# Optimization experiments

Hardware: AMD Instinct MI355X
Metric: run time of the kernel (lower is better)

The kernel has to match this reference:

```python
import jax, jax.numpy as jnp
import numpy as np

B, S = 32, 48
H, W_IMG, DEPTH = 48, 72, 1
UNITS, MOTOR, SENSORY = 48, 4, 1283
ODE_UNFOLDS = 6
N_ACTIONS = 2
EPS = 1e-8


def setup_inputs() -> dict:
    key = jax.random.key(0)
    ks = jax.random.split(key, 32)
    inp = {}
    inp["image"] = jax.random.uniform(ks[0], (B, S, DEPTH, H, W_IMG), jnp.float32)
    inp["rel_pos"] = jax.random.normal(ks[1], (B, S, 3), jnp.float32)
    # CNN params: channels [1->32->64->32], k=3, stride=2, VALID
    dims = [DEPTH, 32, 64, 32]
    for i in range(3):
        fan_in = dims[i] * 9
        inp[f"w{i}"] = jax.random.normal(ks[2 + i], (dims[i + 1], dims[i], 3, 3), jnp.float32) / np.sqrt(fan_in)
        inp[f"b{i}"] = jnp.zeros((dims[i + 1],), jnp.float32)
    # LTC input affine mapping
    inp["input_w"] = jnp.ones((SENSORY,), jnp.float32)
    inp["input_b"] = jnp.zeros((SENSORY,), jnp.float32)
    # LTC neuron params (ncps default init ranges)
    u = lambda k, shp, lo, hi: jax.random.uniform(k, shp, jnp.float32, lo, hi)
    inp["gleak"] = u(ks[6], (UNITS,), 0.001, 1.0)
    inp["vleak"] = u(ks[7], (UNITS,), -0.2, 0.2)
    inp["cm"] = u(ks[8], (UNITS,), 0.4, 0.6)
    # recurrent synapse params [pre=UNITS, post=UNITS]
    inp["sigma"] = u(ks[9], (UNITS, UNITS), 3.0, 8.0)
    inp["mu"] = u(ks[10], (UNITS, UNITS), 0.3, 0.8)
    inp["w_syn"] = u(ks[11], (UNITS, UNITS), 0.001, 1.0)
    inp["erev"] = (2.0 * jax.random.randint(ks[12], (UNITS, UNITS), 0, 2).astype(jnp.float32) - 1.0)
    # sensory synapse params [pre=SENSORY, post=UNITS]
    inp["s_sigma"] = u(ks[13], (SENSORY, UNITS), 3.0, 8.0)
    inp["s_mu"] = u(ks[14], (SENSORY, UNITS), 0.3, 0.8)
    inp["s_w"] = u(ks[15], (SENSORY, UNITS), 0.001, 1.0)
    inp["s_erev"] = (2.0 * jax.random.randint(ks[16], (SENSORY, UNITS), 0, 2).astype(jnp.float32) - 1.0)
    # output affine mapping over the 4 motor neurons
    inp["w_out"] = jnp.ones((MOTOR,), jnp.float32)
    inp["b_out"] = jnp.zeros((MOTOR,), jnp.float32)
    # actor head: Linear(4 -> n_actions) + tanh
    inp["w_head"] = jax.random.normal(ks[17], (MOTOR, N_ACTIONS), jnp.float32) / np.sqrt(MOTOR)
    inp["b_head"] = jnp.zeros((N_ACTIONS,), jnp.float32)
    # sparsity masks (buffers, non-trainable): AutoNCP-like sparse wiring
    inp["syn_mask"] = jax.random.randint(ks[18], (UNITS, UNITS), 0, 2, jnp.int32)
    inp["sens_mask"] = (jax.random.uniform(ks[19], (SENSORY, UNITS)) < 0.4).astype(jnp.int32)
    return inp


def _cnn(x, w0, b0, w1, b1, w2, b2):
    # x: [N, C, H, W], VALID padding, stride 2, ReLU
    for w, b in ((w0, b0), (w1, b1), (w2, b2)):
        x = jax.lax.conv_general_dilated(x, w, (2, 2), "VALID",
                                         dimension_numbers=("NCHW", "OIHW", "NCHW"))
        x = jax.nn.relu(x + b[None, :, None, None])
    return x


def _ltc(xs, input_w, input_b, gleak, vleak, cm, sigma, mu, w_syn, erev,
         s_sigma, s_mu, s_w, s_erev, w_out, b_out, syn_mask_f, sens_mask_f):
    # xs: [B, S, SENSORY] -> outputs [B, S, MOTOR]
    xs = xs * input_w + input_b  # input affine mapping
    cm_t = cm * ODE_UNFOLDS      # cm / (elapsed_time / ode_unfolds), elapsed=1

    def cell(v, x_t):
        # sensory synapse activation, computed once per step: [B, SENSORY, UNITS]
        sa = s_w * jax.nn.sigmoid((x_t[:, :, None] - s_mu) * s_sigma) * sens_mask_f
        w_num_s = jnp.sum(sa * s_erev, axis=1)  # [B, UNITS]
        w_den_s = jnp.sum(sa, axis=1)
        for _ in range(ODE_UNFOLDS):
            # recurrent synapse activation: [B, UNITS(pre), UNITS(post)]
            wa = w_syn * jax.nn.sigmoid((v[:, :, None] - mu) * sigma) * syn_mask_f
            num = cm_t * v + gleak * vleak + jnp.sum(wa * erev, axis=1) + w_num_s
            den = cm_t + gleak + jnp.sum(wa, axis=1) + w_den_s + EPS
            v = num / den
        out = v[:, :MOTOR] * w_out + b_out  # motor neurons + output affine
        return v, out

    v0 = jnp.zeros((xs.shape[0], UNITS), xs.dtype)
    _, outs = jax.lax.scan(cell, v0, jnp.swapaxes(xs, 0, 1))  # scan over time
    return jnp.swapaxes(outs, 0, 1)  # [B, S, MOTOR]


def reference(image, rel_pos, w0, b0, w1, b1, w2, b2, input_w, input_b,
              gleak, vleak, cm, sigma, mu, w_syn, erev,
              s_sigma, s_mu, s_w, s_erev, w_out, b_out, w_head, b_head,
              syn_mask, sens_mask):
    b, s = image.shape[0], image.shape[1]
    img = image.reshape(b * s, *image.shape[2:])
    feat = _cnn(img, w0, b0, w1, b1, w2, b2).reshape(b, s, -1)  # [B,S,1280]
    x = jnp.concatenate([feat, rel_pos.reshape(b, s, -1)], axis=2)  # [B,S,1283]
    outs = _ltc(x, input_w, input_b, gleak, vleak, cm, sigma, mu, w_syn, erev,
                s_sigma, s_mu, s_w, s_erev, w_out, b_out,
                syn_mask.astype(x.dtype), sens_mask.astype(x.dtype))
    pooled = outs.mean(axis=1)  # [B, MOTOR]
    return jnp.tanh(pooled @ w_head + b_head)  # [B, N_ACTIONS]
```

## Files before the change

kernel.cpp:

```cpp
#include <hip/hip_runtime.h>
#include <math.h>

#define DINL __device__ __forceinline__

typedef __attribute__((ext_vector_type(8))) short short8;
typedef __attribute__((ext_vector_type(4))) float f32x4;
typedef unsigned short ushortx;
typedef unsigned int uintx;


static constexpr int O_OUT2 = 0;
static constexpr int O_X    = O_OUT2 + 1536 * 187 * 64;
static constexpr int O_WNUM = O_X + 1536 * 1283;
static constexpr int O_WDEN = O_WNUM + 1536 * 48;
static constexpr int O_SP4  = O_WDEN + 1536 * 48;
static constexpr int O_WM   = O_SP4 + 4 * 48 * 1283;
static constexpr int O_WME  = O_WM + 48 * 48;
static constexpr int O_W2T  = O_WME + 48 * 48;
static constexpr int O_W1H  = O_W2T + 32 * 9 * 64;
static constexpr int O_W1L  = O_W1H + 9216;
static constexpr int O_R4   = O_W1L + 9216;

DINL float sigmoid_f(float z) {
  return __builtin_amdgcn_rcpf(1.f + __expf(-z));
}

DINL ushortx bf16_rne(float x) {
  uintx u = __float_as_uint(x);
  return (ushortx)((u + 0x7FFFu + ((u >> 16) & 1u)) >> 16);
}

__global__ __launch_bounds__(256) void k_pre(
    const float* __restrict__ ssig, const float* __restrict__ smu,
    const float* __restrict__ sw, const float* __restrict__ serev,
    const int* __restrict__ smask,
    const float* __restrict__ w_syn, const float* __restrict__ erev,
    const int* __restrict__ syn_mask,
    const float* __restrict__ gmu, const float* __restrict__ gsig,
    const float* __restrict__ w1, const float* __restrict__ w2,
    float4* __restrict__ o_p4, float4* __restrict__ o_r4,
    float* __restrict__ w2t, ushortx* __restrict__ w1h, ushortx* __restrict__ w1l) {
  const int bid = blockIdx.x, t = threadIdx.x;
  if (bid < 241) {
    int idx = bid * 256 + t;
    if (idx < 61584) {
      int i = idx / 48, j = idx - i * 48;
      float m = (float)smask[idx];
      float w = sw[idx] * m;
      o_p4[j * 1283 + i] = make_float4(ssig[idx], smu[idx], w, w * serev[idx]);
    }
  } else if (bid < 250) {
    int idx = (bid - 241) * 256 + t;
    if (idx < 2304) {
      float wm = w_syn[idx] * (float)syn_mask[idx];
      o_r4[idx] = make_float4(gmu[idx], gsig[idx], wm, wm * erev[idx]);
    }
  } else {
    int idx = (bid - 250) * 256 + t;
    if (idx < 18432) {
      int oc = idx / 288;
      int rem = idx - oc * 288;
      int c = rem / 9, k = rem - c * 9;
      float v = w1[idx];
      ushortx h = bf16_rne(v);
      float hv = __uint_as_float(((uintx)h) << 16);
      ushortx l = bf16_rne(v - hv);
      int dst = (k * 64 + oc) * 32 + c;
      w1h[dst] = h;
      w1l[dst] = l;
    } else if (idx < 36864) {
      int i2 = idx - 18432;
      int oc = i2 / 576;
      int rem = i2 - oc * 576;
      int c = rem / 9, k = rem - c * 9;
      w2t[(((oc & 15) * 9 + k) * 64 + c) * 2 + (oc >> 4)] = w2[i2];
    }
  }
}

__global__ __launch_bounds__(512) void k_conv12(const float* __restrict__ gimg,
        const float* __restrict__ w0, const float* __restrict__ b0,
        const ushortx* __restrict__ w1h, const ushortx* __restrict__ w1l,
        const float* __restrict__ b1, float* __restrict__ gout2) {
  extern __shared__ __align__(16) char dyn[];
  ushortx* c1h = (ushortx*)dyn;
  ushortx* c1l = c1h + 26496;
  float* smem_a = (float*)(c1l + 26496);
  float* sw0 = smem_a + 3456;
  float* sb0 = sw0 + 288;
  ushortx* swh = (ushortx*)smem_a;
  ushortx* swl = swh + 2048;

  const int n = blockIdx.x, t = threadIdx.x;

  const float* gi = gimg + n * 3456;
  for (int k = t; k < 3456; k += 512) smem_a[k] = gi[k];
  if (t < 288) sw0[t] = w0[t];
  if (t >= 480) sb0[t - 480] = b0[t - 480];

  const int lane = t & 63, wid = t >> 6;
  const int r15 = lane & 15, kg = lane >> 4;
  const int mt0 = (wid & 1) * 2;
  const int nt0 = (wid >> 1) * 3;
  int bbase[3], spv[3];
#pragma unroll
  for (int ni = 0; ni < 3; ++ni) {
    int sp = (nt0 + ni) * 16 + r15;
    spv[ni] = sp;
    int spc = sp > 186 ? 186 : sp;
    int oh = spc / 17, ow = spc - oh * 17;
    bbase[ni] = ((2 * oh) * 36 + 2 * ow) * 32 + kg * 8;
  }
  int aoff0 = (mt0 * 16 + r15) * 32 + kg * 8;
  float4 bb[2];
  bb[0] = *(const float4*)(b1 + mt0 * 16 + kg * 4);
  bb[1] = *(const float4*)(b1 + (mt0 + 1) * 16 + kg * 4);
  f32x4 acc[2][3];
#pragma unroll
  for (int mi = 0; mi < 2; ++mi)
#pragma unroll
    for (int ni = 0; ni < 3; ++ni) acc[mi][ni] = (f32x4)(0.f);

  __syncthreads();

  for (int idx = t; idx < 25760; idx += 512) {
    int c = idx & 31, sp = idx >> 5;
    int oh = sp / 35, ow = sp - oh * 35;
    const float* ip = smem_a + (2 * oh) * 72 + 2 * ow;
    const float* wp = sw0 + c * 9;
    float a = sb0[c];
#pragma unroll
    for (int kh = 0; kh < 3; ++kh)
      a += ip[kh * 72 + 0] * wp[kh * 3 + 0] + ip[kh * 72 + 1] * wp[kh * 3 + 1]
         + ip[kh * 72 + 2] * wp[kh * 3 + 2];
    a = fmaxf(a, 0.f);
    ushortx h = bf16_rne(a);
    float hv = __uint_as_float(((uintx)h) << 16);
    ushortx l = bf16_rne(a - hv);
    int pos = (oh * 36 + ow) * 32 + c;
    c1h[pos] = h;
    c1l[pos] = l;
  }

  const uintx* gwh = (const uintx*)w1h;
  const uintx* gwl = (const uintx*)w1l;
  for (int tap = 0; tap < 9; ++tap) {
    __syncthreads();
    for (int k = t; k < 1024; k += 512) {
      ((uintx*)swh)[k] = gwh[tap * 1024 + k];
      ((uintx*)swl)[k] = gwl[tap * 1024 + k];
    }
    __syncthreads();
    const int kh = tap / 3, kw = tap - kh * 3;
    const int toff = (kh * 36 + kw) * 32;
    short8 ah[2], al[2];
    ah[0] = *(const short8*)(swh + aoff0);
    al[0] = *(const short8*)(swl + aoff0);
    ah[1] = *(const short8*)(swh + aoff0 + 512);
    al[1] = *(const short8*)(swl + aoff0 + 512);
#pragma unroll
    for (int ni = 0; ni < 3; ++ni) {
      short8 bh = *(const short8*)(c1h + bbase[ni] + toff);
      short8 bl = *(const short8*)(c1l + bbase[ni] + toff);
#pragma unroll
      for (int mi = 0; mi < 2; ++mi) {
        acc[mi][ni] = __builtin_amdgcn_mfma_f32_16x16x32_bf16(ah[mi], bh, acc[mi][ni], 0, 0, 0);
        acc[mi][ni] = __builtin_amdgcn_mfma_f32_16x16x32_bf16(al[mi], bh, acc[mi][ni], 0, 0, 0);
        acc[mi][ni] = __builtin_amdgcn_mfma_f32_16x16x32_bf16(ah[mi], bl, acc[mi][ni], 0, 0, 0);
      }
    }
  }

  float* go = gout2 + n * 11968;
#pragma unroll
  for (int mi = 0; mi < 2; ++mi)
#pragma unroll
    for (int ni = 0; ni < 3; ++ni) {
      if (spv[ni] < 187) {
        float4 v;
        v.x = fmaxf(acc[mi][ni][0] + bb[mi].x, 0.f);
        v.y = fmaxf(acc[mi][ni][1] + bb[mi].y, 0.f);
        v.z = fmaxf(acc[mi][ni][2] + bb[mi].z, 0.f);
        v.w = fmaxf(acc[mi][ni][3] + bb[mi].w, 0.f);
        *(float4*)(go + spv[ni] * 64 + (mt0 + mi) * 16 + kg * 4) = v;
      }
    }
}

__global__ __launch_bounds__(256, 4) void k_conv3(const float* __restrict__ gout2,
        const float* __restrict__ w2t, const float* __restrict__ b2,
        const float* __restrict__ grel, float* __restrict__ gx) {
  __shared__ __align__(16) float sin2g[16 * 198];
  __shared__ __align__(16) float sw2g[16 * 290];
  const int n = blockIdx.x, t = threadIdx.x;
  const float* gi = gout2 + n * 11968;

  const int oc = t & 15, g = t >> 4;
  float acc[3][2];
  int rowb[3];
#pragma unroll
  for (int q = 0; q < 3; ++q) {
    acc[q][0] = b2[oc]; acc[q][1] = b2[oc + 16];
    int sp = q * 16 + g; if (sp > 39) sp = 39;
    int oh = sp >> 3, ow = sp & 7;
    rowb[q] = (2 * oh) * 18 + 2 * ow;
  }

  for (int grp = 0; grp < 4; ++grp) {
    for (int idx = t; idx < 2992; idx += 256) {
      int sp = idx >> 4, c = idx & 15;
      int h = sp / 17, w = sp - h * 17;
      sin2g[c * 198 + h * 18 + w] = gi[sp * 64 + grp * 16 + c];
    }
    for (int idx = t; idx < 4608; idx += 256) {
      int ocq2 = idx / 288, r = idx - ocq2 * 288;
      int k = r >> 5;
      sw2g[ocq2 * 290 + r] = w2t[(ocq2 * 9 + k) * 128 + grp * 32 + (r & 31)];
    }
    __syncthreads();

    for (int c = 0; c < 16; ++c) {
      const float* cb = sin2g + c * 198;
      const float* wb = sw2g + oc * 290 + c * 2;
#pragma unroll
      for (int kh = 0; kh < 3; ++kh) {
        float2 wv0 = *(const float2*)(wb + (kh * 3 + 0) * 32);
        float2 wv1 = *(const float2*)(wb + (kh * 3 + 1) * 32);
        float2 wv2 = *(const float2*)(wb + (kh * 3 + 2) * 32);
#pragma unroll
        for (int q = 0; q < 3; ++q) {
          const float* p = cb + rowb[q] + kh * 18;
          float2 x01 = *(const float2*)p;
          float x2 = p[2];
          acc[q][0] += x01.x * wv0.x + x01.y * wv1.x + x2 * wv2.x;
          acc[q][1] += x01.x * wv0.y + x01.y * wv1.y + x2 * wv2.y;
        }
      }
    }
    __syncthreads();
  }

  float* xo = gx + n * 1283;
#pragma unroll
  for (int q = 0; q < 3; ++q) {
    int sp = q * 16 + g;
    if (sp < 40) {
      xo[oc * 40 + sp]        = fmaxf(acc[q][0], 0.f);
      xo[(oc + 16) * 40 + sp] = fmaxf(acc[q][1], 0.f);
    }
  }
  if (t < 3) xo[1280 + t] = grel[n * 3 + t];
}

__global__ __launch_bounds__(256) void k_sensory(const float* __restrict__ gx,
        const float* __restrict__ iw, const float* __restrict__ ib,
        const float4* __restrict__ p4,
        float* __restrict__ wnum, float* __restrict__ wden) {
  __shared__ float xs[4 * 1283];
  const int t = threadIdx.x, bid = blockIdx.x;
  const int bs0 = (bid >> 1) * 4;
  const int jbase = (bid & 1) * 24;
  for (int idx = t; idx < 4 * 1283; idx += 256) {
    int slot = idx / 1283, i = idx - slot * 1283;
    xs[idx] = gx[(bs0 + slot) * 1283 + i] * iw[i] + ib[i];
  }
  __syncthreads();
  const int w = t >> 6, l = t & 63;
  for (int jj = 0; jj < 6; ++jj) {
    int j = jbase + w * 6 + jj;
    const float4* pp = p4 + j * 1283;
    float an[4], ad[4];
#pragma unroll
    for (int s2 = 0; s2 < 4; ++s2) { an[s2] = 0.f; ad[s2] = 0.f; }
    for (int i = l; i < 1283; i += 64) {
      float4 P = pp[i];
#pragma unroll
      for (int s2 = 0; s2 < 4; ++s2) {
        float sg = sigmoid_f((xs[s2 * 1283 + i] - P.y) * P.x);
        an[s2] += P.w * sg;
        ad[s2] += P.z * sg;
      }
    }
#pragma unroll
    for (int off = 32; off; off >>= 1)
#pragma unroll
      for (int s2 = 0; s2 < 4; ++s2) {
        an[s2] += __shfl_xor(an[s2], off);
        ad[s2] += __shfl_xor(ad[s2], off);
      }
    if (l == 0) {
#pragma unroll
      for (int s2 = 0; s2 < 4; ++s2) {
        wnum[(bs0 + s2) * 48 + j] = an[s2];
        wden[(bs0 + s2) * 48 + j] = ad[s2];
      }
    }
  }
}

__global__ __launch_bounds__(192) void k_scan(const float4* __restrict__ r4,
        const float* __restrict__ wnum, const float* __restrict__ wden,
        const float* __restrict__ gleak, const float* __restrict__ vleak,
        const float* __restrict__ cm,
        const float* __restrict__ w_out, const float* __restrict__ b_out,
        const float* __restrict__ w_head, const float* __restrict__ b_head,
        float* __restrict__ out) {
  __shared__ float swn[48 * 48], swd[48 * 48];
  __shared__ __align__(16) float vbuf[2][48];
  __shared__ float m4[4];
  const int t = threadIdx.x, b = blockIdx.x;
  const int j = t >> 2, g = t & 3;

  const float* gn = wnum + b * 2304;
  const float* gd = wden + b * 2304;
  for (int k = t; k < 2304; k += 192) { swn[k] = gn[k]; swd[k] = gd[k]; }

  float4 P[12];
#pragma unroll
  for (int q = 0; q < 12; ++q) P[q] = r4[(g * 12 + q) * 48 + j];

  const float cmt = cm[j] * 6.f;
  const float gl = gleak[j];
  const float glv = gl * vleak[j];
  if (t < 48) { vbuf[0][t] = 0.f; vbuf[1][t] = 0.f; }
  float psum = 0.f;
  __syncthreads();

  int cur = 0;
  for (int s = 0; s < 48; ++s) {
    float wns = swn[s * 48 + j], wds = swd[s * 48 + j];
#pragma unroll 1
    for (int u = 0; u < 6; ++u) {
      const float4* vb4 = (const float4*)&vbuf[cur][g * 12];
      float4 va = vb4[0], vb = vb4[1], vc = vb4[2];
      float vv[12] = {va.x, va.y, va.z, va.w, vb.x, vb.y, vb.z, vb.w,
                      vc.x, vc.y, vc.z, vc.w};
      float an = 0.f, ad = 0.f;
#pragma unroll
      for (int q = 0; q < 12; ++q) {
        float sg = sigmoid_f((vv[q] - P[q].x) * P[q].y);
        an += P[q].w * sg;
        ad += P[q].z * sg;
      }
      an += __shfl_xor(an, 1); ad += __shfl_xor(ad, 1);
      an += __shfl_xor(an, 2); ad += __shfl_xor(ad, 2);
      if (g == 0) {
        float vj = vbuf[cur][j];
        float num = cmt * vj + glv + an + wns;
        float den = cmt + gl + ad + wds + 1e-8f;
        vbuf[cur ^ 1][j] = num / den;
      }
      __syncthreads();
      cur ^= 1;
    }
    if (g == 0 && j < 4) psum += vbuf[cur][j];
  }
  if (g == 0 && j < 4) m4[j] = psum * (1.f / 48.f) * w_out[j] + b_out[j];
  __syncthreads();
  if (t < 2) {
    float a = b_head[t];
#pragma unroll
    for (int jm = 0; jm < 4; ++jm) a += m4[jm] * w_head[jm * 2 + t];
    out[b * 2 + t] = tanhf(a);
  }
}

extern "C" void kernel_launch(void* const* d_in, const int* in_sizes, int n_in,
                              void* d_out, int out_size, void* d_ws, size_t ws_size,
                              hipStream_t stream) {
  const float* image   = (const float*)d_in[0];
  const float* rel     = (const float*)d_in[1];
  const float* w0      = (const float*)d_in[2];
  const float* b0      = (const float*)d_in[3];
  const float* w1      = (const float*)d_in[4];
  const float* b1      = (const float*)d_in[5];
  const float* w2      = (const float*)d_in[6];
  const float* b2      = (const float*)d_in[7];
  const float* iw      = (const float*)d_in[8];
  const float* ib      = (const float*)d_in[9];
  const float* gleak   = (const float*)d_in[10];
  const float* vleak   = (const float*)d_in[11];
  const float* cm      = (const float*)d_in[12];
  const float* sigma   = (const float*)d_in[13];
  const float* mu      = (const float*)d_in[14];
  const float* w_syn   = (const float*)d_in[15];
  const float* erev    = (const float*)d_in[16];
  const float* s_sigma = (const float*)d_in[17];
  const float* s_mu    = (const float*)d_in[18];
  const float* s_w     = (const float*)d_in[19];
  const float* s_erev  = (const float*)d_in[20];
  const float* w_out   = (const float*)d_in[21];
  const float* b_out   = (const float*)d_in[22];
  const float* w_head  = (const float*)d_in[23];
  const float* b_head  = (const float*)d_in[24];
  const int* syn_mask  = (const int*)d_in[25];
  const int* sens_mask = (const int*)d_in[26];
  float* ws  = (float*)d_ws;
  float* out = (float*)d_out;

  hipFuncSetAttribute((const void*)k_conv12,
                      hipFuncAttributeMaxDynamicSharedMemorySize, 131072);

  k_pre<<<394, 256, 0, stream>>>(s_sigma, s_mu, s_w, s_erev, sens_mask,
      w_syn, erev, syn_mask, mu, sigma, w1, w2,
      (float4*)(ws + O_SP4), (float4*)(ws + O_R4), ws + O_W2T,
      (ushortx*)(ws + O_W1H), (ushortx*)(ws + O_W1L));

  k_conv12<<<1536, 512, 121088, stream>>>(image, w0, b0,
      (const ushortx*)(ws + O_W1H), (const ushortx*)(ws + O_W1L), b1, ws + O_OUT2);
  k_conv3<<<1536, 256, 0, stream>>>(ws + O_OUT2, ws + O_W2T, b2, rel, ws + O_X);

  k_sensory<<<768, 256, 0, stream>>>(ws + O_X, iw, ib,
      (const float4*)(ws + O_SP4), ws + O_WNUM, ws + O_WDEN);

  k_scan<<<32, 192, 0, stream>>>((const float4*)(ws + O_R4),
      ws + O_WNUM, ws + O_WDEN, gleak, vleak, cm,
      w_out, b_out, w_head, b_head, out);
}
```

Baseline: 512.0 us.

## Fuse conv3 into CNN kernel with split-bf16 MFMA and single-wave scan

Conv3 is merged into the conv1/conv2 kernel. The conv2 output stays in LDS as hi/lo bf16 pairs and is consumed by a split-bf16 MFMA conv3, so the global round trip of the large intermediate is gone. LDS indexing is XOR-swizzled to reduce bank conflicts, and conv2 weights are now read straight from global memory instead of being staged per tap. The LTC scan is rewritten to use one wavefront per batch, passing state through shuffles instead of LDS and barriers, which trades per-step sync cost for more work per thread and a possible accuracy change from the 3-term bf16 split.

```diff
diff --git a/kernel.cpp b/kernel.cpp
--- a/kernel.cpp
+++ b/kernel.cpp
@@ -4,22 +4,21 @@
 #define DINL __device__ __forceinline__
 
 typedef __attribute__((ext_vector_type(8))) short short8;
+typedef __attribute__((ext_vector_type(4))) short short4x;
 typedef __attribute__((ext_vector_type(4))) float f32x4;
 typedef unsigned short ushortx;
 typedef unsigned int uintx;
 
 
-static constexpr int O_OUT2 = 0;
-static constexpr int O_X    = O_OUT2 + 1536 * 187 * 64;
+static constexpr int O_X    = 0;
 static constexpr int O_WNUM = O_X + 1536 * 1283;
 static constexpr int O_WDEN = O_WNUM + 1536 * 48;
 static constexpr int O_SP4  = O_WDEN + 1536 * 48;
-static constexpr int O_WM   = O_SP4 + 4 * 48 * 1283;
-static constexpr int O_WME  = O_WM + 48 * 48;
-static constexpr int O_W2T  = O_WME + 48 * 48;
-static constexpr int O_W1H  = O_W2T + 32 * 9 * 64;
+static constexpr int O_W1H  = O_SP4 + 4 * 48 * 1283;
 static constexpr int O_W1L  = O_W1H + 9216;
-static constexpr int O_R4   = O_W1L + 9216;
+static constexpr int O_W3H  = O_W1L + 9216;
+static constexpr int O_W3L  = O_W3H + 9216;
+static constexpr int O_R4   = O_W3L + 9216;
 
 DINL float sigmoid_f(float z) {
   return __builtin_amdgcn_rcpf(1.f + __expf(-z));
@@ -29,6 +28,8 @@
   uintx u = __float_as_uint(x);
   return (ushortx)((u + 0x7FFFu + ((u >> 16) & 1u)) >> 16);
 }
+
+DINL int swz(int sp, int idx) { return idx ^ (((sp >> 1) & 7) << 3); }
 
 __global__ __launch_bounds__(256) void k_pre(
     const float* __restrict__ ssig, const float* __restrict__ smu,
@@ -39,7 +40,8 @@
     const float* __restrict__ gmu, const float* __restrict__ gsig,
     const float* __restrict__ w1, const float* __restrict__ w2,
     float4* __restrict__ o_p4, float4* __restrict__ o_r4,
-    float* __restrict__ w2t, ushortx* __restrict__ w1h, ushortx* __restrict__ w1l) {
+    ushortx* __restrict__ w1h, ushortx* __restrict__ w1l,
+    ushortx* __restrict__ w3h, ushortx* __restrict__ w3l) {
   const int bid = blockIdx.x, t = threadIdx.x;
   if (bid < 241) {
     int idx = bid * 256 + t;
@@ -66,35 +68,42 @@
       float hv = __uint_as_float(((uintx)h) << 16);
       ushortx l = bf16_rne(v - hv);
       int dst = (k * 64 + oc) * 32 + c;
-      w1h[dst] = h;
-      w1l[dst] = l;
+      w1h[dst] = h; w1l[dst] = l;
     } else if (idx < 36864) {
       int i2 = idx - 18432;
       int oc = i2 / 576;
       int rem = i2 - oc * 576;
       int c = rem / 9, k = rem - c * 9;
-      w2t[(((oc & 15) * 9 + k) * 64 + c) * 2 + (oc >> 4)] = w2[i2];
-    }
-  }
-}
-
-__global__ __launch_bounds__(512) void k_conv12(const float* __restrict__ gimg,
+      float v = w2[i2];
+      ushortx h = bf16_rne(v);
+      float hv = __uint_as_float(((uintx)h) << 16);
+      ushortx l = bf16_rne(v - hv);
+      int dst = (k * 32 + oc) * 64 + c;
+      w3h[dst] = h; w3l[dst] = l;
+    }
+  }
+}
+
+__global__ __launch_bounds__(512) void k_cnn(const float* __restrict__ gimg,
         const float* __restrict__ w0, const float* __restrict__ b0,
         const ushortx* __restrict__ w1h, const ushortx* __restrict__ w1l,
-        const float* __restrict__ b1, float* __restrict__ gout2) {
+        const float* __restrict__ b1,
+        const ushortx* __restrict__ w3h, const ushortx* __restrict__ w3l,
+        const float* __restrict__ b2,
+        const float* __restrict__ grel, float* __restrict__ gx) {
   extern __shared__ __align__(16) char dyn[];
   ushortx* c1h = (ushortx*)dyn;
   ushortx* c1l = c1h + 26496;
-  float* smem_a = (float*)(c1l + 26496);
-  float* sw0 = smem_a + 3456;
+  float* simg = (float*)(c1l + 26496);
+  float* sw0 = simg + 3456;
   float* sb0 = sw0 + 288;
-  ushortx* swh = (ushortx*)smem_a;
-  ushortx* swl = swh + 2048;
+  ushortx* o2h = c1h;
+  ushortx* o2l = c1l;
 
   const int n = blockIdx.x, t = threadIdx.x;
 
   const float* gi = gimg + n * 3456;
-  for (int k = t; k < 3456; k += 512) smem_a[k] = gi[k];
+  for (int k = t; k < 3456; k += 512) simg[k] = gi[k];
   if (t < 288) sw0[t] = w0[t];
   if (t >= 480) sb0[t - 480] = b0[t - 480];
 
@@ -102,16 +111,15 @@
   const int r15 = lane & 15, kg = lane >> 4;
   const int mt0 = (wid & 1) * 2;
   const int nt0 = (wid >> 1) * 3;
-  int bbase[3], spv[3];
+  int b36[3], spv[3];
 #pragma unroll
   for (int ni = 0; ni < 3; ++ni) {
     int sp = (nt0 + ni) * 16 + r15;
     spv[ni] = sp;
     int spc = sp > 186 ? 186 : sp;
     int oh = spc / 17, ow = spc - oh * 17;
-    bbase[ni] = ((2 * oh) * 36 + 2 * ow) * 32 + kg * 8;
-  }
-  int aoff0 = (mt0 * 16 + r15) * 32 + kg * 8;
+    b36[ni] = (2 * oh) * 36 + 2 * ow;
+  }
   float4 bb[2];
   bb[0] = *(const float4*)(b1 + mt0 * 16 + kg * 4);
   bb[1] = *(const float4*)(b1 + (mt0 + 1) * 16 + kg * 4);
@@ -126,7 +134,7 @@
   for (int idx = t; idx < 25760; idx += 512) {
     int c = idx & 31, sp = idx >> 5;
     int oh = sp / 35, ow = sp - oh * 35;
-    const float* ip = smem_a + (2 * oh) * 72 + 2 * ow;
+    const float* ip = simg + (2 * oh) * 72 + 2 * ow;
     const float* wp = sw0 + c * 9;
     float a = sb0[c];
 #pragma unroll
@@ -137,31 +145,28 @@
     ushortx h = bf16_rne(a);
     float hv = __uint_as_float(((uintx)h) << 16);
     ushortx l = bf16_rne(a - hv);
-    int pos = (oh * 36 + ow) * 32 + c;
+    int sp36 = oh * 36 + ow;
+    int pos = swz(sp36, sp36 * 32 + c);
     c1h[pos] = h;
     c1l[pos] = l;
   }
-
-  const uintx* gwh = (const uintx*)w1h;
-  const uintx* gwl = (const uintx*)w1l;
+  __syncthreads();
+
   for (int tap = 0; tap < 9; ++tap) {
-    __syncthreads();
-    for (int k = t; k < 1024; k += 512) {
-      ((uintx*)swh)[k] = gwh[tap * 1024 + k];
-      ((uintx*)swl)[k] = gwl[tap * 1024 + k];
-    }
-    __syncthreads();
     const int kh = tap / 3, kw = tap - kh * 3;
-    const int toff = (kh * 36 + kw) * 32;
     short8 ah[2], al[2];
-    ah[0] = *(const short8*)(swh + aoff0);
-    al[0] = *(const short8*)(swl + aoff0);
-    ah[1] = *(const short8*)(swh + aoff0 + 512);
-    al[1] = *(const short8*)(swl + aoff0 + 512);
+#pragma unroll
+    for (int mi = 0; mi < 2; ++mi) {
+      int aoff = (tap * 64 + (mt0 + mi) * 16 + r15) * 32 + kg * 8;
+      ah[mi] = *(const short8*)(w1h + aoff);
+      al[mi] = *(const short8*)(w1l + aoff);
+    }
 #pragma unroll
     for (int ni = 0; ni < 3; ++ni) {
-      short8 bh = *(const short8*)(c1h + bbase[ni] + toff);
-      short8 bl = *(const short8*)(c1l + bbase[ni] + toff);
+      int sp36 = b36[ni] + kh * 36 + kw;
+      int bidx = swz(sp36, sp36 * 32 + kg * 8);
+      short8 bh = *(const short8*)(c1h + bidx);
+      short8 bl = *(const short8*)(c1l + bidx);
 #pragma unroll
       for (int mi = 0; mi < 2; ++mi) {
         acc[mi][ni] = __builtin_amdgcn_mfma_f32_16x16x32_bf16(ah[mi], bh, acc[mi][ni], 0, 0, 0);
@@ -171,85 +176,61 @@
     }
   }
 
-  float* go = gout2 + n * 11968;
+  __syncthreads();
+
 #pragma unroll
   for (int mi = 0; mi < 2; ++mi)
 #pragma unroll
     for (int ni = 0; ni < 3; ++ni) {
       if (spv[ni] < 187) {
-        float4 v;
-        v.x = fmaxf(acc[mi][ni][0] + bb[mi].x, 0.f);
-        v.y = fmaxf(acc[mi][ni][1] + bb[mi].y, 0.f);
-        v.z = fmaxf(acc[mi][ni][2] + bb[mi].z, 0.f);
-        v.w = fmaxf(acc[mi][ni][3] + bb[mi].w, 0.f);
-        *(float4*)(go + spv[ni] * 64 + (mt0 + mi) * 16 + kg * 4) = v;
-      }
-    }
-}
-
-__global__ __launch_bounds__(256, 4) void k_conv3(const float* __restrict__ gout2,
-        const float* __restrict__ w2t, const float* __restrict__ b2,
-        const float* __restrict__ grel, float* __restrict__ gx) {
-  __shared__ __align__(16) float sin2g[16 * 198];
-  __shared__ __align__(16) float sw2g[16 * 290];
-  const int n = blockIdx.x, t = threadIdx.x;
-  const float* gi = gout2 + n * 11968;
-
-  const int oc = t & 15, g = t >> 4;
-  float acc[3][2];
-  int rowb[3];
-#pragma unroll
-  for (int q = 0; q < 3; ++q) {
-    acc[q][0] = b2[oc]; acc[q][1] = b2[oc + 16];
-    int sp = q * 16 + g; if (sp > 39) sp = 39;
-    int oh = sp >> 3, ow = sp & 7;
-    rowb[q] = (2 * oh) * 18 + 2 * ow;
-  }
-
-  for (int grp = 0; grp < 4; ++grp) {
-    for (int idx = t; idx < 2992; idx += 256) {
-      int sp = idx >> 4, c = idx & 15;
-      int h = sp / 17, w = sp - h * 17;
-      sin2g[c * 198 + h * 18 + w] = gi[sp * 64 + grp * 16 + c];
-    }
-    for (int idx = t; idx < 4608; idx += 256) {
-      int ocq2 = idx / 288, r = idx - ocq2 * 288;
-      int k = r >> 5;
-      sw2g[ocq2 * 290 + r] = w2t[(ocq2 * 9 + k) * 128 + grp * 32 + (r & 31)];
-    }
-    __syncthreads();
-
-    for (int c = 0; c < 16; ++c) {
-      const float* cb = sin2g + c * 198;
-      const float* wb = sw2g + oc * 290 + c * 2;
-#pragma unroll
-      for (int kh = 0; kh < 3; ++kh) {
-        float2 wv0 = *(const float2*)(wb + (kh * 3 + 0) * 32);
-        float2 wv1 = *(const float2*)(wb + (kh * 3 + 1) * 32);
-        float2 wv2 = *(const float2*)(wb + (kh * 3 + 2) * 32);
-#pragma unroll
-        for (int q = 0; q < 3; ++q) {
-          const float* p = cb + rowb[q] + kh * 18;
-          float2 x01 = *(const float2*)p;
-          float x2 = p[2];
-          acc[q][0] += x01.x * wv0.x + x01.y * wv1.x + x2 * wv2.x;
-          acc[q][1] += x01.x * wv0.y + x01.y * wv1.y + x2 * wv2.y;
+        short4x h4, l4;
+#pragma unroll
+        for (int r = 0; r < 4; ++r) {
+          float v = fmaxf(acc[mi][ni][r] + ((const float*)&bb[mi])[r], 0.f);
+          ushortx h = bf16_rne(v);
+          float hv = __uint_as_float(((uintx)h) << 16);
+          h4[r] = (short)h;
+          l4[r] = (short)bf16_rne(v - hv);
         }
-      }
-    }
-    __syncthreads();
-  }
-
-  float* xo = gx + n * 1283;
-#pragma unroll
-  for (int q = 0; q < 3; ++q) {
-    int sp = q * 16 + g;
-    if (sp < 40) {
-      xo[oc * 40 + sp]        = fmaxf(acc[q][0], 0.f);
-      xo[(oc + 16) * 40 + sp] = fmaxf(acc[q][1], 0.f);
-    }
-  }
-  if (t < 3) xo[1280 + t] = grel[n * 3 + t];
+        int base = swz(spv[ni], spv[ni] * 64 + (mt0 + mi) * 16 + kg * 4);
+        *(short4x*)(o2h + base) = h4;
+        *(short4x*)(o2l + base) = l4;
+      }
+    }
+  __syncthreads();
+
+  if (wid < 6) {
+    const int mt = wid & 1, nt = wid >> 1;
+    int sp_out = nt * 16 + r15;
+    int spc3 = sp_out > 39 ? 39 : sp_out;
+    int oh3 = spc3 >> 3, ow3 = spc3 & 7;
+    f32x4 a3 = (f32x4)(0.f);
+    for (int tap = 0; tap < 9; ++tap) {
+      const int kh = tap / 3, kw = tap - kh * 3;
+      int sp_in = (2 * oh3 + kh) * 17 + (2 * ow3 + kw);
+#pragma unroll
+      for (int ks = 0; ks < 2; ++ks) {
+        int aoff = (tap * 32 + mt * 16 + r15) * 64 + ks * 32 + kg * 8;
+        short8 ah3 = *(const short8*)(w3h + aoff);
+        short8 al3 = *(const short8*)(w3l + aoff);
+        int bidx = swz(sp_in, sp_in * 64 + ks * 32 + kg * 8);
+        short8 bh = *(const short8*)(o2h + bidx);
+        short8 bl = *(const short8*)(o2l + bidx);
+        a3 = __builtin_amdgcn_mfma_f32_16x16x32_bf16(ah3, bh, a3, 0, 0, 0);
+        a3 = __builtin_amdgcn_mfma_f32_16x16x32_bf16(al3, bh, a3, 0, 0, 0);
+        a3 = __builtin_amdgcn_mfma_f32_16x16x32_bf16(ah3, bl, a3, 0, 0, 0);
+      }
+    }
+    if (sp_out < 40) {
+      float* xo = gx + n * 1283;
+#pragma unroll
+      for (int r = 0; r < 4; ++r) {
+        int oc = mt * 16 + kg * 4 + r;
+        xo[oc * 40 + sp_out] = fmaxf(a3[r] + b2[oc], 0.f);
+      }
+    }
+  }
+  if (t < 3) gx[n * 1283 + 1280 + t] = grel[n * 3 + t];
 }
 
 __global__ __launch_bounds__(256) void k_sensory(const float* __restrict__ gx,
@@ -298,69 +279,86 @@
   }
 }
 
-__global__ __launch_bounds__(192) void k_scan(const float4* __restrict__ r4,
+__global__ __launch_bounds__(64) void k_scan(const float4* __restrict__ r4,
         const float* __restrict__ wnum, const float* __restrict__ wden,
         const float* __restrict__ gleak, const float* __restrict__ vleak,
         const float* __restrict__ cm,
         const float* __restrict__ w_out, const float* __restrict__ b_out,
         const float* __restrict__ w_head, const float* __restrict__ b_head,
         float* __restrict__ out) {
-  __shared__ float swn[48 * 48], swd[48 * 48];
-  __shared__ __align__(16) float vbuf[2][48];
-  __shared__ float m4[4];
+  __shared__ float swn[2304], swd[2304];
   const int t = threadIdx.x, b = blockIdx.x;
-  const int j = t >> 2, g = t & 3;
+  const int j16 = t & 15, q = t >> 4;
 
   const float* gn = wnum + b * 2304;
   const float* gd = wden + b * 2304;
-  for (int k = t; k < 2304; k += 192) { swn[k] = gn[k]; swd[k] = gd[k]; }
-
-  float4 P[12];
-#pragma unroll
-  for (int q = 0; q < 12; ++q) P[q] = r4[(g * 12 + q) * 48 + j];
-
-  const float cmt = cm[j] * 6.f;
-  const float gl = gleak[j];
-  const float glv = gl * vleak[j];
-  if (t < 48) { vbuf[0][t] = 0.f; vbuf[1][t] = 0.f; }
+  for (int k = t; k < 2304; k += 64) { swn[k] = gn[k]; swd[k] = gd[k]; }
+
+  float4 P[3][12];
+  float cmt[3], gl[3], glv[3];
+#pragma unroll
+  for (int p = 0; p < 3; ++p) {
+    int j = j16 + 16 * p;
+#pragma unroll
+    for (int k = 0; k < 12; ++k) P[p][k] = r4[(12 * q + k) * 48 + j];
+    cmt[p] = cm[j] * 6.f;
+    gl[p] = gleak[j];
+    glv[p] = gl[p] * vleak[j];
+  }
+  float v0 = 0.f, v1 = 0.f, v2 = 0.f;
   float psum = 0.f;
   __syncthreads();
 
-  int cur = 0;
   for (int s = 0; s < 48; ++s) {
-    float wns = swn[s * 48 + j], wds = swd[s * 48 + j];
+    float wns[3], wds[3];
+#pragma unroll
+    for (int p = 0; p < 3; ++p) {
+      wns[p] = swn[s * 48 + j16 + 16 * p];
+      wds[p] = swd[s * 48 + j16 + 16 * p];
+    }
 #pragma unroll 1
     for (int u = 0; u < 6; ++u) {
-      const float4* vb4 = (const float4*)&vbuf[cur][g * 12];
-      float4 va = vb4[0], vb = vb4[1], vc = vb4[2];
-      float vv[12] = {va.x, va.y, va.z, va.w, vb.x, vb.y, vb.z, vb.w,
-                      vc.x, vc.y, vc.z, vc.w};
-      float an = 0.f, ad = 0.f;
-#pragma unroll
-      for (int q = 0; q < 12; ++q) {
-        float sg = sigmoid_f((vv[q] - P[q].x) * P[q].y);
-        an += P[q].w * sg;
-        ad += P[q].z * sg;
-      }
-      an += __shfl_xor(an, 1); ad += __shfl_xor(ad, 1);
-      an += __shfl_xor(an, 2); ad += __shfl_xor(ad, 2);
-      if (g == 0) {
-        float vj = vbuf[cur][j];
-        float num = cmt * vj + glv + an + wns;
-        float den = cmt + gl + ad + wds + 1e-8f;
-        vbuf[cur ^ 1][j] = num / den;
-      }
-      __syncthreads();
-      cur ^= 1;
-    }
-    if (g == 0 && j < 4) psum += vbuf[cur][j];
-  }
-  if (g == 0 && j < 4) m4[j] = psum * (1.f / 48.f) * w_out[j] + b_out[j];
-  __syncthreads();
+      float vsub = (q == 0) ? v0 : ((q == 1) ? v1 : v2);
+      float vv[12];
+#pragma unroll
+      for (int k = 0; k < 12; ++k) vv[k] = __shfl(vsub, 12 * q + k);
+      float an[3] = {0.f, 0.f, 0.f}, ad[3] = {0.f, 0.f, 0.f};
+#pragma unroll
+      for (int p = 0; p < 3; ++p)
+#pragma unroll
+        for (int k = 0; k < 12; ++k) {
+          float4 Pp = P[p][k];
+          float e = __expf((Pp.x - vv[k]) * Pp.y);
+          float sg = __builtin_amdgcn_rcpf(1.f + e);
+          an[p] += Pp.w * sg;
+          ad[p] += Pp.z * sg;
+        }
+#pragma unroll
+      for (int p = 0; p < 3; ++p) {
+        an[p] += __shfl_xor(an[p], 16); ad[p] += __shfl_xor(ad[p], 16);
+        an[p] += __shfl_xor(an[p], 32); ad[p] += __shfl_xor(ad[p], 32);
+      }
+      float vn[3];
+#pragma unroll
+      for (int p = 0; p < 3; ++p) {
+        float num = cmt[p] * ((p == 0) ? v0 : (p == 1) ? v1 : v2) + glv[p] + an[p] + wns[p];
+        float den = cmt[p] + gl[p] + ad[p] + wds[p] + 1e-8f;
+        float r = __builtin_amdgcn_rcpf(den);
+        r = r * (2.f - den * r);
+        vn[p] = num * r;
+      }
+      v0 = vn[0]; v1 = vn[1]; v2 = vn[2];
+    }
+    psum += v0;
+  }
+  float m = psum * (1.f / 48.f);
+  float m0 = __shfl(m, 0), m1 = __shfl(m, 1), m2 = __shfl(m, 2), m3 = __shfl(m, 3);
   if (t < 2) {
     float a = b_head[t];
-#pragma unroll
-    for (int jm = 0; jm < 4; ++jm) a += m4[jm] * w_head[jm * 2 + t];
+    a += (m0 * w_out[0] + b_out[0]) * w_head[0 * 2 + t];
+    a += (m1 * w_out[1] + b_out[1]) * w_head[1 * 2 + t];
+    a += (m2 * w_out[2] + b_out[2]) * w_head[2 * 2 + t];
+    a += (m3 * w_out[3] + b_out[3]) * w_head[3 * 2 + t];
     out[b * 2 + t] = tanhf(a);
   }
 }
@@ -398,22 +396,24 @@
   float* ws  = (float*)d_ws;
   float* out = (float*)d_out;
 
-  hipFuncSetAttribute((const void*)k_conv12,
+  hipFuncSetAttribute((const void*)k_cnn,
                       hipFuncAttributeMaxDynamicSharedMemorySize, 131072);
 
   k_pre<<<394, 256, 0, stream>>>(s_sigma, s_mu, s_w, s_erev, sens_mask,
       w_syn, erev, syn_mask, mu, sigma, w1, w2,
-      (float4*)(ws + O_SP4), (float4*)(ws + O_R4), ws + O_W2T,
-      (ushortx*)(ws + O_W1H), (ushortx*)(ws + O_W1L));
-
-  k_conv12<<<1536, 512, 121088, stream>>>(image, w0, b0,
-      (const ushortx*)(ws + O_W1H), (const ushortx*)(ws + O_W1L), b1, ws + O_OUT2);
-  k_conv3<<<1536, 256, 0, stream>>>(ws + O_OUT2, ws + O_W2T, b2, rel, ws + O_X);
+      (float4*)(ws + O_SP4), (float4*)(ws + O_R4),
+      (ushortx*)(ws + O_W1H), (ushortx*)(ws + O_W1L),
+      (ushortx*)(ws + O_W3H), (ushortx*)(ws + O_W3L));
+
+  k_cnn<<<1536, 512, 121088, stream>>>(image, w0, b0,
+      (const ushortx*)(ws + O_W1H), (const ushortx*)(ws + O_W1L), b1,
+      (const ushortx*)(ws + O_W3H), (const ushortx*)(ws + O_W3L), b2,
+      rel, ws + O_X);
 
   k_sensory<<<768, 256, 0, stream>>>(ws + O_X, iw, ib,
       (const float4*)(ws + O_SP4), ws + O_WNUM, ws + O_WDEN);
 
-  k_scan<<<32, 192, 0, stream>>>((const float4*)(ws + O_R4),
+  k_scan<<<32, 64, 0, stream>>>((const float4*)(ws + O_R4),
       ws + O_WNUM, ws + O_WDEN, gleak, vleak, cm,
       w_out, b_out, w_head, b_head, out);
 }
```

New measurement: 535.9 us. 1.05x slower.
